# Performance work log

Hardware: AMD Instinct MI355X
Metric: run time of the kernel (lower is better)

## Reference

```python
import jax, jax.numpy as jnp
import numpy as np

N_HEAD, D_HEAD = 16, 64
D_MODEL = N_HEAD * D_HEAD
QLEN, MLEN, BSZ = 1024, 1024, 4
KLEN = QLEN + MLEN
LN_EPS = 1e-5


def setup_inputs() -> dict:
    key = jax.random.key(0)
    ks = jax.random.split(key, 8)
    w = jax.random.normal(ks[0], (QLEN, BSZ, D_MODEL), jnp.float32)
    r = jax.random.normal(ks[1], (KLEN, D_MODEL), jnp.float32)
    mems = jax.random.normal(ks[2], (MLEN, BSZ, D_MODEL), jnp.float32)
    # causal mask over (qlen, klen): query i may attend keys j <= i + MLEN
    i = jnp.arange(QLEN)[:, None]
    j = jnp.arange(KLEN)[None, :]
    attn_mask = j > (i + MLEN)  # True = masked
    s = 1.0 / np.sqrt(D_MODEL)
    qkv_w = jax.random.normal(ks[3], (3 * D_MODEL, D_MODEL), jnp.float32) * s
    r_net_w = jax.random.normal(ks[4], (D_MODEL, D_MODEL), jnp.float32) * s
    o_w = jax.random.normal(ks[5], (D_MODEL, D_MODEL), jnp.float32) * s
    r_r_bias = jax.random.normal(ks[6], (N_HEAD, D_HEAD), jnp.float32) * 0.02
    r_w_bias = jax.random.normal(ks[7], (N_HEAD, D_HEAD), jnp.float32) * 0.02
    ln_gamma = jnp.ones((D_MODEL,), jnp.float32)
    ln_beta = jnp.zeros((D_MODEL,), jnp.float32)
    return {"w": w, "r": r, "mems": mems, "attn_mask": attn_mask,
            "qkv_w": qkv_w, "r_net_w": r_net_w, "o_w": o_w,
            "r_r_bias": r_r_bias, "r_w_bias": r_w_bias,
            "ln_gamma": ln_gamma, "ln_beta": ln_beta}


def _layer_norm(x, g, b):
    mu = jnp.mean(x, axis=-1, keepdims=True)
    var = jnp.var(x, axis=-1, keepdims=True)
    return (x - mu) * jax.lax.rsqrt(var + LN_EPS) * g + b


def _rel_shift(x):
    # x: [qlen, rlen, bsz, n_head]
    q, rl, b, n = x.shape
    x_pad = jnp.pad(x, ((0, 0), (1, 0), (0, 0), (0, 0)))  # zero row at front of axis 1
    x_pad = x_pad.reshape(rl + 1, q, b, n)
    return x_pad[1:].reshape(q, rl, b, n)


def reference(w, r, mems, attn_mask, qkv_w, r_net_w, o_w, r_r_bias, r_w_bias, ln_gamma, ln_beta):
    qlen, bsz = w.shape[0], w.shape[1]
    cat = jnp.concatenate([mems, w], axis=0)  # [klen, b, d]
    klen = cat.shape[0]
    w_heads = cat @ qkv_w.T  # [klen, b, 3*d]
    r_head_k = (r @ r_net_w.T).reshape(r.shape[0], N_HEAD, D_HEAD)  # [rlen, n, dh]
    w_q, w_k, w_v = jnp.split(w_heads, 3, axis=-1)
    w_q = w_q[-qlen:].reshape(qlen, bsz, N_HEAD, D_HEAD)
    w_k = w_k.reshape(klen, bsz, N_HEAD, D_HEAD)
    w_v = w_v.reshape(klen, bsz, N_HEAD, D_HEAD)

    scale = 1.0 / np.sqrt(D_HEAD)
    AC = jnp.einsum('ibnd,jbnd->ijbn', w_q + r_w_bias, w_k)
    BD = _rel_shift(jnp.einsum('ibnd,jnd->ijbn', w_q + r_r_bias, r_head_k))
    attn_score = (AC + BD) * scale
    attn_score = jnp.where(attn_mask[None, :, :, None].transpose(1, 2, 0, 3), -1e30, attn_score) if False else \
        jnp.where(attn_mask[:, :, None, None], jnp.float32(-1e30), attn_score)
    attn_prob = jax.nn.softmax(attn_score, axis=1)
    attn_vec = jnp.einsum('ijbn,jbnd->ibnd', attn_prob, w_v)
    attn_vec = attn_vec.reshape(qlen, bsz, N_HEAD * D_HEAD)
    attn_out = attn_vec @ o_w.T
    return _layer_norm(w + attn_out, ln_gamma, ln_beta)
```

## Files before the change

kernel.cpp:

```cpp
#include <hip/hip_runtime.h>
#include <hip/hip_bf16.h>

typedef __attribute__((ext_vector_type(8))) short short8;
typedef __attribute__((ext_vector_type(4))) float f32x4;
typedef __hip_bfloat16 bf16;

#define NHEAD 16
#define DHEAD 64
#define DMODEL 1024
#define QLEN 1024
#define MLEN 1024
#define BSZ 4
#define KLEN 2048
#define LOG2E 1.44269504088896f

__device__ __forceinline__ float fast_exp2(float x) {
#if __has_builtin(__builtin_amdgcn_exp2f)
  return __builtin_amdgcn_exp2f(x);
#else
  return exp2f(x);
#endif
}

__device__ __forceinline__ short8 ld8(const bf16* p) { return *(const short8*)p; }
__device__ __forceinline__ void st8(bf16* p, short8 v) { *(short8*)p = v; }
__device__ __forceinline__ f32x4 mfma16(short8 a, short8 b, f32x4 c) {
  return __builtin_amdgcn_mfma_f32_16x16x32_bf16(a, b, c, 0, 0, 0);
}
__device__ __forceinline__ float bfu2f(unsigned short u) {
  unsigned int x = ((unsigned int)u) << 16;
  return __uint_as_float(x);
}
__device__ __forceinline__ unsigned short f2bfu(float f) {
  bf16 t = __float2bfloat16(f);
  return *(unsigned short*)&t;
}
__device__ __forceinline__ unsigned short f2bfu_fast(float f) {
  return (unsigned short)((__float_as_uint(f) + 0x8000u) >> 16);
}
__device__ __forceinline__ bf16 bf16_raw(unsigned short u) {
  bf16 t; *(unsigned short*)&t = u; return t;
}
__device__ __forceinline__ void async16(const bf16* g, bf16* l) {
  __builtin_amdgcn_global_load_lds(
      (const __attribute__((address_space(1))) unsigned int*)g,
      (__attribute__((address_space(3))) unsigned int*)l, 16, 0, 0);
}

#define DPPF(x, ctrl, rm) \
  __int_as_float(__builtin_amdgcn_update_dpp( \
      __float_as_int(x), __float_as_int(x), (ctrl), (rm), 0xF, false))

__global__ void detect_dtype(const unsigned short* wq, int* flag) {
  const int tid = threadIdx.x;
  int cnt = 0;
  #pragma unroll
  for (int j = 0; j < 8; ++j) {
    unsigned short u = wq[2 * (tid * 8 + j)];
    int e = (u >> 7) & 0xFF;
    if (e >= 100 && e <= 134) cnt++;
  }
  #pragma unroll
  for (int o = 32; o > 0; o >>= 1) cnt += __shfl_xor(cnt, o, 64);
  __shared__ int red[4];
  if ((tid & 63) == 0) red[tid >> 6] = cnt;
  __syncthreads();
  if (tid == 0) {
    int total = red[0] + red[1] + red[2] + red[3];
    *flag = (total > 1024) ? 0 : 1;
  }
}

__global__ __launch_bounds__(256) void convert_inputs(
    const void* s0, const void* s1, const void* s2,
    const void* s3, const void* s4, const void* s5,
    bf16* d0, bf16* d1, bf16* d2, bf16* d3, bf16* d4, bf16* d5,
    const int* flag)
{
  const int b = blockIdx.x;
  const void* src; bf16* dst; int lb;
  if (b < 2048)      { src = s0; dst = d0; lb = b; }
  else if (b < 4096) { src = s1; dst = d1; lb = b - 2048; }
  else if (b < 5120) { src = s2; dst = d2; lb = b - 4096; }
  else if (b < 6656) { src = s3; dst = d3; lb = b - 5120; }
  else if (b < 7168) { src = s4; dst = d4; lb = b - 6656; }
  else               { src = s5; dst = d5; lb = b - 7168; }
  const size_t idx = ((size_t)lb * 256 + threadIdx.x) * 8;
  if (*flag) {
    const float* f = (const float*)src;
    short8 v;
    #pragma unroll
    for (int j = 0; j < 8; ++j) v[j] = (short)f2bfu(f[idx + j]);
    st8(dst + idx, v);
  } else {
    st8(dst + idx, ld8((const bf16*)src + idx));
  }
}

__device__ __forceinline__ void gemm_core64(
    const bf16* const ap[4], const bf16* const bp[4],
    bf16* As, bf16* Bs, int wv, int wm, int wn, int lr, int lg,
    f32x4 acc[4][4])
{
  const int sx = lr & 7;
  for (int k0 = 0; k0 < DMODEL; k0 += 64) {
    #pragma unroll
    for (int p = 0; p < 4; ++p) {
      async16(ap[p] + k0, As + (wv * 32 + p * 8) * 64);
      async16(bp[p] + k0, Bs + (wv * 32 + p * 8) * 64);
    }
    __syncthreads();
    #pragma unroll
    for (int ks = 0; ks < 2; ++ks) {
      const int col = (((ks * 4 + lg) ^ sx) << 3);
      short8 af[4], bfr[4];
      #pragma unroll
      for (int mt = 0; mt < 4; ++mt) af[mt] = ld8(As + (wm * 64 + mt * 16 + lr) * 64 + col);
      #pragma unroll
      for (int nt = 0; nt < 4; ++nt) bfr[nt] = ld8(Bs + (wn * 64 + nt * 16 + lr) * 64 + col);
      #pragma unroll
      for (int mt = 0; mt < 4; ++mt)
        #pragma unroll
        for (int nt = 0; nt < 4; ++nt)
          acc[mt][nt] = mfma16(af[mt], bfr[nt], acc[mt][nt]);
    }
    __syncthreads();
  }
}

__global__ __launch_bounds__(256) void qkv_gemm(
    const bf16* __restrict__ w, const bf16* __restrict__ mems,
    const bf16* __restrict__ qkv_w,
    const bf16* __restrict__ r, const bf16* __restrict__ rnet_w,
    const void* __restrict__ r_w_bias, const void* __restrict__ r_r_bias,
    const int* __restrict__ flag,
    bf16* __restrict__ qac, bf16* __restrict__ qbd,
    bf16* __restrict__ kbuf, bf16* __restrict__ vbuf,
    bf16* __restrict__ rkbuf)
{
  const int id = blockIdx.x;
  int sec, bx, by;
  if (id < 256)       { sec = 0; bx = id >> 5;                    by = 32 + (id & 31); }
  else if (id < 768)  { sec = 1; int t = id - 256;  bx = 8  + (t >> 6); by = t & 63; }
  else if (id < 1280) { sec = 2; int t = id - 768;  bx = 16 + (t >> 6); by = t & 63; }
  else                { sec = 3; int t = id - 1280; bx = 24 + (t >> 4); by = t & 15; }
  __shared__ bf16 sh[16384];
  bf16* As = sh;
  bf16* Bs = sh + 8192;
  const int tid = threadIdx.x;
  const int lane = tid & 63, wv = tid >> 6;
  const int wm = wv >> 1, wn = wv & 1;
  const int lr = lane & 15, lg = lane >> 4;
  const int lr8 = lane >> 3;
  const int ucol = ((lane & 7) ^ lr8) * 8;
  const bf16 *ap[4], *bp[4];
  #pragma unroll
  for (int p = 0; p < 4; ++p) {
    int arow = wv * 32 + p * 8 + lr8;
    if (sec == 3) {
      ap[p] = r + (size_t)(by * 128 + arow) * DMODEL + ucol;
      bp[p] = rnet_w + (size_t)((bx - 24) * 128 + arow) * DMODEL + ucol;
    } else {
      int m = by * 128 + arow;
      int j = m >> 2, b = m & 3;
      ap[p] = ((j < MLEN) ? (mems + ((size_t)(j * BSZ + b)) * DMODEL)
                          : (w + ((size_t)((j - MLEN) * BSZ + b)) * DMODEL)) + ucol;
      bp[p] = qkv_w + (size_t)(bx * 128 + arow) * DMODEL + ucol;
    }
  }
  f32x4 zero = {0.f, 0.f, 0.f, 0.f};
  f32x4 acc[4][4];
  #pragma unroll
  for (int a = 0; a < 4; ++a)
    #pragma unroll
    for (int c2 = 0; c2 < 4; ++c2) acc[a][c2] = zero;
  gemm_core64(ap, bp, As, Bs, wv, wm, wn, lr, lg, acc);

  if (sec == 2) {
    #pragma unroll
    for (int nt = 0; nt < 4; ++nt) {
      int n = wn * 64 + nt * 16 + lr;
      #pragma unroll
      for (int mt = 0; mt < 4; ++mt) {
        int jl = wm * 16 + mt * 4 + lg;
        #pragma unroll
        for (int rr = 0; rr < 4; ++rr) {
          int x = rr * 32 + jl;
          sh[n * 128 + (((x >> 4) ^ (n & 7)) << 4) + (x & 15)] =
              __float2bfloat16(acc[mt][nt][rr]);
        }
      }
    }
    __syncthreads();
    const int grp = lane >> 3, sl = lane & 7;
    const int hbase = (bx - 16) * 2;
    #pragma unroll
    for (int i = 0; i < 16; ++i) {
      int idx = i * 32 + wv * 8 + grp;
      int n = idx >> 2, bb = idx & 3;
      int x0 = bb * 32 + sl * 4;
      ushort4 v4 = *(const ushort4*)(sh + n * 128 + (((x0 >> 4) ^ (n & 7)) << 4) + (x0 & 15));
      int hh = hbase + (n >> 6), dd = n & 63;
      *(ushort4*)(vbuf + ((size_t)(bb * NHEAD + hh) * DHEAD + dd) * KLEN + by * 32 + sl * 4) = v4;
    }
    return;
  }
  if (sec == 3) {
    #pragma unroll
    for (int nt = 0; nt < 4; ++nt) {
      int col = (bx - 24) * 128 + wn * 64 + nt * 16 + lr;
      int h = col >> 6, d = col & 63;
      #pragma unroll
      for (int mt = 0; mt < 4; ++mt) {
        #pragma unroll
        for (int rr = 0; rr < 4; ++rr) {
          int m = by * 128 + wm * 64 + mt * 16 + lg * 4 + rr;
          rkbuf[((size_t)h * KLEN + m) * DHEAD + d] = __float2bfloat16(acc[mt][nt][rr]);
        }
      }
    }
    return;
  }
  const int isf = (sec == 0) ? *flag : 0;
  const float QSC = 0.125f * LOG2E;
  #pragma unroll
  for (int nt = 0; nt < 4; ++nt) {
    int col = bx * 128 + wn * 64 + nt * 16 + lr;
    int nn = col & 1023;
    int h = nn >> 6, d = nn & 63;
    float rwb = 0.f, rrb = 0.f;
    if (sec == 0) {
      if (isf) { rwb = ((const float*)r_w_bias)[nn]; rrb = ((const float*)r_r_bias)[nn]; }
      else { rwb = __bfloat162float(((const bf16*)r_w_bias)[nn]);
             rrb = __bfloat162float(((const bf16*)r_r_bias)[nn]); }
    }
    #pragma unroll
    for (int mt = 0; mt < 4; ++mt) {
      #pragma unroll
      for (int rr = 0; rr < 4; ++rr) {
        int m = by * 128 + wm * 64 + mt * 16 + lg * 4 + rr;
        int j = m >> 2, b = m & 3;
        float v = acc[mt][nt][rr];
        if (sec == 0) {
          int i = j - MLEN;
          size_t base = (((size_t)(b * NHEAD + h)) * QLEN + i) * DHEAD + d;
          qac[base] = __float2bfloat16((v + rwb) * QSC);
          qbd[base] = __float2bfloat16((v + rrb) * QSC);
        } else {
          kbuf[(((size_t)(b * NHEAD + h)) * KLEN + j) * DHEAD + d] = __float2bfloat16(v);
        }
      }
    }
  }
}

#define RRBODY(RR, CTRL) { \
    const int di = g * 4 + RR; \
    float sh[5]; \
    _Pragma("unroll") for (int ct = 0; ct < 5; ++ct) { \
      float y = Gr[ct][RR]; \
      sh[ct] = __int_as_float(__builtin_amdgcn_update_dpp( \
          __float_as_int(y), __float_as_int(y), (CTRL), 0xF, 0xF, false)); \
    } \
    float sv[4]; \
    _Pragma("unroll") for (int jt = 0; jt < 4; ++jt) { \
      float bd = (c > di) ? sh[jt + 1] : sh[jt]; \
      sv[jt] = S[jt][RR] + bd; \
    } \
    if (lastt) { \
      const int ig = i0 + wv * 16 + di; \
      _Pragma("unroll") for (int jt = 0; jt < 4; ++jt) \
        if (j0 + jt * 16 + c > ig + MLEN) sv[jt] = -1e30f; \
    } \
    _Pragma("unroll") for (int jt = 0; jt < 4; ++jt) { \
      float pv = fast_exp2(sv[jt]); \
      ls[RR] += pv; \
      pw[di * 64 + ((((jt * 2) + (c >> 3)) ^ (di & 7)) << 3) + (c & 7)] = \
          bf16_raw(f2bfu_fast(pv)); \
    } \
  }

__global__ __launch_bounds__(256, 4) void attn_kernel(
    const bf16* __restrict__ qac, const bf16* __restrict__ qbd,
    const bf16* __restrict__ kbuf, const bf16* __restrict__ vbuf,
    const bf16* __restrict__ rkbuf, bf16* __restrict__ av)
{
  const int id = blockIdx.x;
  const int qt = 15 - (id >> 6);
  const int bh = id & 63;
  const int b = bh >> 4, h = bh & 15;
  const int i0 = qt * 64;
  __shared__ bf16 Ks[64 * 64];
  __shared__ bf16 Vt[64 * 64];
  __shared__ bf16 Rs[128 * 64];
  __shared__ bf16 Ps[4 * 16 * 64];
  const int tid = threadIdx.x;
  const int wv = tid >> 6, lane = tid & 63;
  const int c = lane & 15, g = lane >> 4;
  const size_t bhb = (size_t)(b * NHEAD + h);
  const int lr8 = lane >> 3;
  const int ucol = ((lane & 7) ^ lr8) * 8;
  const int sw0 = ((0 + g) ^ (c & 7)) * 8;
  const int sw1 = ((4 + g) ^ (c & 7)) * 8;

  short8 qaf[2], qbf[2];
  {
    const size_t qrow = (bhb * QLEN + i0 + wv * 16 + c) * DHEAD;
    #pragma unroll
    for (int ks = 0; ks < 2; ++ks) {
      qaf[ks] = ld8(qac + qrow + ks * 32 + g * 8);
      qbf[ks] = ld8(qbd + qrow + ks * 32 + g * 8);
    }
  }
  f32x4 zero = {0.f, 0.f, 0.f, 0.f};
  f32x4 O[4];
  #pragma unroll
  for (int dt = 0; dt < 4; ++dt) O[dt] = zero;
  float ls[4] = {0.f, 0.f, 0.f, 0.f};

  bf16* pw = Ps + wv * (16 * 64);
  const bf16* kc = Ks + c * 64;
  const bf16* vc = Vt + c * 64;
  const bf16* rc = Rs + (c + 48 - wv * 16) * 64;
  const int ntiles = qt + 17;
  for (int t = 0; t < ntiles; ++t) {
    const int j0 = t * 64;
    const int m_lo = j0 - i0 + 960;
    #pragma unroll
    for (int p = 0; p < 2; ++p) {
      int r0 = wv * 16 + p * 8;
      async16(kbuf + (bhb * KLEN + j0 + r0 + lr8) * DHEAD + ucol, Ks + r0 * 64);
      async16(vbuf + (bhb * DHEAD + r0 + lr8) * KLEN + j0 + ucol, Vt + r0 * 64);
    }
    #pragma unroll
    for (int p = 0; p < 4; ++p) {
      int r0 = wv * 32 + p * 8;
      async16(rkbuf + ((size_t)h * KLEN + m_lo + r0 + lr8) * DHEAD + ucol, Rs + r0 * 64);
    }
    __syncthreads();
    f32x4 S[4], G[5];
    #pragma unroll
    for (int jt = 0; jt < 4; ++jt) S[jt] = zero;
    #pragma unroll
    for (int ct = 0; ct < 5; ++ct) G[ct] = zero;
    #pragma unroll
    for (int ks = 0; ks < 2; ++ks) {
      const int sw = ks ? sw1 : sw0;
      #pragma unroll
      for (int jt = 0; jt < 4; ++jt)
        S[jt] = mfma16(qaf[ks], ld8(kc + jt * 1024 + sw), S[jt]);
      #pragma unroll
      for (int ct = 0; ct < 5; ++ct)
        G[ct] = mfma16(qbf[ks], ld8(rc + ct * 1024 + sw), G[ct]);
    }
    float Gr[5][4];
    #pragma unroll
    for (int ct = 0; ct < 5; ++ct)
      #pragma unroll
      for (int rr = 0; rr < 4; ++rr) {
        float y = G[ct][rr];
        y = DPPF(y, 0x124, 0xE);
        y = DPPF(y, 0x124, 0xC);
        y = DPPF(y, 0x124, 0x8);
        Gr[ct][rr] = y;
      }
    const bool lastt = (t == ntiles - 1);
    RRBODY(0, 0x121)
    RRBODY(1, 0x122)
    RRBODY(2, 0x123)
    RRBODY(3, 0x124)
    #pragma unroll
    for (int ks = 0; ks < 2; ++ks) {
      short8 pf = ld8(pw + c * 64 + (((ks * 4 + g) ^ (c & 7)) << 3));
      const int sw = ks ? sw1 : sw0;
      #pragma unroll
      for (int dt = 0; dt < 4; ++dt)
        O[dt] = mfma16(pf, ld8(vc + dt * 1024 + sw), O[dt]);
    }
    __syncthreads();
  }
  #pragma unroll
  for (int rr = 0; rr < 4; ++rr) {
    float s = ls[rr];
    s += DPPF(s, 0xB1, 0xF);
    s += DPPF(s, 0x4E, 0xF);
    s += DPPF(s, 0x141, 0xF);
    s += DPPF(s, 0x140, 0xF);
    ls[rr] = s;
  }
  #pragma unroll
  for (int rr = 0; rr < 4; ++rr) {
    float inv = 1.0f / ls[rr];
    #pragma unroll
    for (int dt = 0; dt < 4; ++dt) {
      int ig = i0 + wv * 16 + g * 4 + rr;
      int d = dt * 16 + c;
      av[((size_t)ig * BSZ + b) * DMODEL + h * DHEAD + d] =
          __float2bfloat16(O[dt][rr] * inv);
    }
  }
}

__global__ __launch_bounds__(256) void out_gemm(
    const bf16* __restrict__ av, const bf16* __restrict__ o_w,
    bf16* __restrict__ ao)
{
  const int id = blockIdx.x;
  const int bx = id >> 5, by = id & 31;
  __shared__ bf16 As[128 * 64];
  __shared__ bf16 Bs[128 * 64];
  const int tid = threadIdx.x;
  const int lane = tid & 63, wv = tid >> 6;
  const int wm = wv >> 1, wn = wv & 1;
  const int lr = lane & 15, lg = lane >> 4;
  const int lr8 = lane >> 3;
  const int ucol = ((lane & 7) ^ lr8) * 8;
  const bf16 *ap[4], *bp[4];
  #pragma unroll
  for (int p = 0; p < 4; ++p) {
    int arow = wv * 32 + p * 8 + lr8;
    ap[p] = av + (size_t)(by * 128 + arow) * DMODEL + ucol;
    bp[p] = o_w + (size_t)(bx * 128 + arow) * DMODEL + ucol;
  }
  f32x4 zero = {0.f, 0.f, 0.f, 0.f};
  f32x4 acc[4][4];
  #pragma unroll
  for (int a = 0; a < 4; ++a)
    #pragma unroll
    for (int c2 = 0; c2 < 4; ++c2) acc[a][c2] = zero;
  gemm_core64(ap, bp, As, Bs, wv, wm, wn, lr, lg, acc);
  #pragma unroll
  for (int nt = 0; nt < 4; ++nt) {
    int col = bx * 128 + wn * 64 + nt * 16 + lr;
    #pragma unroll
    for (int mt = 0; mt < 4; ++mt) {
      #pragma unroll
      for (int rr = 0; rr < 4; ++rr) {
        int m = by * 128 + wm * 64 + mt * 16 + lg * 4 + rr;
        ao[(size_t)m * DMODEL + col] = __float2bfloat16(acc[mt][nt][rr]);
      }
    }
  }
}

__global__ __launch_bounds__(256) void ln_kernel(
    const void* __restrict__ wz, const bf16* __restrict__ ao,
    const void* __restrict__ gz, const void* __restrict__ bz,
    void* __restrict__ outz, const int* __restrict__ flag)
{
  const int m = blockIdx.x;
  const int tid = threadIdx.x;
  const int isf = *flag;
  ushort4 au = ((const ushort4*)ao)[m * 256 + tid];
  float a4[4];
  a4[0] = bfu2f(au.x); a4[1] = bfu2f(au.y); a4[2] = bfu2f(au.z); a4[3] = bfu2f(au.w);
  float x[4], gg[4], bb[4];
  if (isf) {
    f32x4 w4 = ((const f32x4*)wz)[m * 256 + tid];
    f32x4 g4 = ((const f32x4*)gz)[tid];
    f32x4 b4 = ((const f32x4*)bz)[tid];
    #pragma unroll
    for (int k = 0; k < 4; ++k) { x[k] = w4[k] + a4[k]; gg[k] = g4[k]; bb[k] = b4[k]; }
  } else {
    ushort4 w4 = ((const ushort4*)wz)[m * 256 + tid];
    ushort4 g4 = ((const ushort4*)gz)[tid];
    ushort4 b4 = ((const ushort4*)bz)[tid];
    x[0] = bfu2f(w4.x) + a4[0]; x[1] = bfu2f(w4.y) + a4[1];
    x[2] = bfu2f(w4.z) + a4[2]; x[3] = bfu2f(w4.w) + a4[3];
    gg[0] = bfu2f(g4.x); gg[1] = bfu2f(g4.y); gg[2] = bfu2f(g4.z); gg[3] = bfu2f(g4.w);
    bb[0] = bfu2f(b4.x); bb[1] = bfu2f(b4.y); bb[2] = bfu2f(b4.z); bb[3] = bfu2f(b4.w);
  }
  float s = x[0] + x[1] + x[2] + x[3];
  float s2 = x[0]*x[0] + x[1]*x[1] + x[2]*x[2] + x[3]*x[3];
  #pragma unroll
  for (int o = 32; o > 0; o >>= 1) {
    s += __shfl_xor(s, o, 64);
    s2 += __shfl_xor(s2, o, 64);
  }
  __shared__ float red[8];
  const int wv = tid >> 6, lane = tid & 63;
  if (lane == 0) { red[wv] = s; red[4 + wv] = s2; }
  __syncthreads();
  s = red[0] + red[1] + red[2] + red[3];
  s2 = red[4] + red[5] + red[6] + red[7];
  const float mu = s * (1.0f / DMODEL);
  const float var = s2 * (1.0f / DMODEL) - mu * mu;
  const float rstd = rsqrtf(var + 1e-5f);
  float y[4];
  #pragma unroll
  for (int k = 0; k < 4; ++k) y[k] = (x[k] - mu) * rstd * gg[k] + bb[k];
  if (isf) {
    f32x4 o4; o4[0] = y[0]; o4[1] = y[1]; o4[2] = y[2]; o4[3] = y[3];
    ((f32x4*)outz)[m * 256 + tid] = o4;
  } else {
    ushort4 o4;
    o4.x = f2bfu(y[0]); o4.y = f2bfu(y[1]); o4.z = f2bfu(y[2]); o4.w = f2bfu(y[3]);
    ((ushort4*)outz)[m * 256 + tid] = o4;
  }
}

extern "C" void kernel_launch(void* const* d_in, const int* in_sizes, int n_in,
                              void* d_out, int out_size, void* d_ws, size_t ws_size,
                              hipStream_t stream) {
  (void)in_sizes; (void)n_in; (void)out_size; (void)ws_size;
  const void* w      = d_in[0];
  const void* r      = d_in[1];
  const void* mems   = d_in[2];
  const void* qkv_w  = d_in[4];
  const void* rnet_w = d_in[5];
  const void* o_w    = d_in[6];
  const void* rrb    = d_in[7];
  const void* rwb    = d_in[8];
  const void* ln_g   = d_in[9];
  const void* ln_b   = d_in[10];

  char* ws = (char*)d_ws;
  const size_t MB = 1ull << 20;
  bf16* cw    = (bf16*)(ws + 0 * MB);
  bf16* cmems = (bf16*)(ws + 8 * MB);
  bf16* cr    = (bf16*)(ws + 16 * MB);
  bf16* cqkvw = (bf16*)(ws + 20 * MB);
  bf16* crnet = (bf16*)(ws + 26 * MB);
  bf16* cow   = (bf16*)(ws + 28 * MB);
  int*  flag  = (int*)(ws + 30 * MB);
  bf16* qac   = (bf16*)(ws + 31 * MB);
  bf16* qbd   = (bf16*)(ws + 39 * MB);
  bf16* kbuf  = (bf16*)(ws + 47 * MB);
  bf16* vbuf  = (bf16*)(ws + 63 * MB);
  bf16* rkbuf = (bf16*)(ws + 79 * MB);
  bf16* av    = (bf16*)(ws + 83 * MB);
  bf16* ao    = (bf16*)(ws + 0 * MB);

  detect_dtype<<<1, 256, 0, stream>>>((const unsigned short*)w, flag);
  convert_inputs<<<7680, 256, 0, stream>>>(w, mems, r, qkv_w, rnet_w, o_w,
                                           cw, cmems, cr, cqkvw, crnet, cow, flag);
  qkv_gemm<<<1408, 256, 0, stream>>>(cw, cmems, cqkvw, cr, crnet,
                                     rwb, rrb, flag,
                                     qac, qbd, kbuf, vbuf, rkbuf);
  attn_kernel<<<1024, 256, 0, stream>>>(qac, qbd, kbuf, vbuf, rkbuf, av);
  out_gemm<<<256, 256, 0, stream>>>(av, cow, ao);
  ln_kernel<<<dim3(4096), 256, 0, stream>>>(w, ao, ln_g, ln_b, d_out, flag);
}
```

Baseline: 307.0 us.

## Reuse overlapping R tile via ring buffer and overlap R loads with QK MFMAs

The relative-position R window slides by 64 rows per key tile, so the loop now keeps 128 rows in LDS as a ring indexed by an XOR offset. After the first tile it loads only the 64 new rows, and the wait on them is moved so the QK MFMAs run while they arrive. The DPP row-shift chain is cut from three steps to two, and the fp32→bf16 convert uses vector loads. The cost is more complex waitcnt/barrier handling and a split MFMA phase with an extra barrier.

New measurement: 299.9 us. -2.3%, faster.

```diff
diff --git a/kernel.cpp b/kernel.cpp
--- a/kernel.cpp
+++ b/kernel.cpp
@@ -87,10 +87,14 @@
   else               { src = s5; dst = d5; lb = b - 7168; }
   const size_t idx = ((size_t)lb * 256 + threadIdx.x) * 8;
   if (*flag) {
-    const float* f = (const float*)src;
+    const f32x4* f = (const f32x4*)src;
+    f32x4 a = f[idx >> 2];
+    f32x4 c = f[(idx >> 2) + 1];
     short8 v;
-    #pragma unroll
-    for (int j = 0; j < 8; ++j) v[j] = (short)f2bfu(f[idx + j]);
+    v[0] = (short)f2bfu(a[0]); v[1] = (short)f2bfu(a[1]);
+    v[2] = (short)f2bfu(a[2]); v[3] = (short)f2bfu(a[3]);
+    v[4] = (short)f2bfu(c[0]); v[5] = (short)f2bfu(c[1]);
+    v[6] = (short)f2bfu(c[2]); v[7] = (short)f2bfu(c[3]);
     st8(dst + idx, v);
   } else {
     st8(dst + idx, ld8((const bf16*)src + idx));
@@ -321,23 +325,45 @@
   bf16* pw = Ps + wv * (16 * 64);
   const bf16* kc = Ks + c * 64;
   const bf16* vc = Vt + c * 64;
-  const bf16* rc = Rs + (c + 48 - wv * 16) * 64;
+  const int relb = c + 48 - wv * 16;
+  int relo[2][5];
+  #pragma unroll
+  for (int ks = 0; ks < 2; ++ks)
+    #pragma unroll
+    for (int ct = 0; ct < 5; ++ct)
+      relo[ks][ct] = (relb + ct * 16) * 64 + (ks ? sw1 : sw0);
+
   const int ntiles = qt + 17;
+  int roff = ((15 - qt) & 1) << 6;
   for (int t = 0; t < ntiles; ++t) {
     const int j0 = t * 64;
     const int m_lo = j0 - i0 + 960;
+    const int ro = roff << 6;
     #pragma unroll
     for (int p = 0; p < 2; ++p) {
       int r0 = wv * 16 + p * 8;
       async16(kbuf + (bhb * KLEN + j0 + r0 + lr8) * DHEAD + ucol, Ks + r0 * 64);
       async16(vbuf + (bhb * DHEAD + r0 + lr8) * KLEN + j0 + ucol, Vt + r0 * 64);
     }
-    #pragma unroll
-    for (int p = 0; p < 4; ++p) {
-      int r0 = wv * 32 + p * 8;
-      async16(rkbuf + ((size_t)h * KLEN + m_lo + r0 + lr8) * DHEAD + ucol, Rs + r0 * 64);
-    }
-    __syncthreads();
+    if (t == 0) {
+      #pragma unroll
+      for (int p = 0; p < 4; ++p) {
+        int r0 = wv * 32 + p * 8;
+        async16(rkbuf + ((size_t)h * KLEN + m_lo + r0 + lr8) * DHEAD + ucol,
+                Rs + ((r0 << 6) ^ ro));
+      }
+      asm volatile("s_waitcnt vmcnt(4)" ::: "memory");
+    } else {
+      #pragma unroll
+      for (int p = 0; p < 2; ++p) {
+        int r1 = 64 + wv * 16 + p * 8;
+        async16(rkbuf + ((size_t)h * KLEN + m_lo + r1 + lr8) * DHEAD + ucol,
+                Rs + ((r1 << 6) ^ ro));
+      }
+      asm volatile("s_waitcnt vmcnt(2)" ::: "memory");
+    }
+    __builtin_amdgcn_s_barrier();
+    __builtin_amdgcn_sched_barrier(0);
     f32x4 S[4], G[5];
     #pragma unroll
     for (int jt = 0; jt < 4; ++jt) S[jt] = zero;
@@ -349,9 +375,15 @@
       #pragma unroll
       for (int jt = 0; jt < 4; ++jt)
         S[jt] = mfma16(qaf[ks], ld8(kc + jt * 1024 + sw), S[jt]);
+    }
+    __builtin_amdgcn_sched_barrier(0);
+    asm volatile("s_waitcnt vmcnt(0)" ::: "memory");
+    __syncthreads();
+    #pragma unroll
+    for (int ks = 0; ks < 2; ++ks) {
       #pragma unroll
       for (int ct = 0; ct < 5; ++ct)
-        G[ct] = mfma16(qbf[ks], ld8(rc + ct * 1024 + sw), G[ct]);
+        G[ct] = mfma16(qbf[ks], ld8(Rs + (relo[ks][ct] ^ ro)), G[ct]);
     }
     float Gr[5][4];
     #pragma unroll
@@ -359,9 +391,8 @@
       #pragma unroll
       for (int rr = 0; rr < 4; ++rr) {
         float y = G[ct][rr];
-        y = DPPF(y, 0x124, 0xE);
-        y = DPPF(y, 0x124, 0xC);
-        y = DPPF(y, 0x124, 0x8);
+        y = DPPF(y, 0x124, 0xA);
+        y = DPPF(y, 0x128, 0xC);
         Gr[ct][rr] = y;
       }
     const bool lastt = (t == ntiles - 1);
@@ -378,6 +409,7 @@
         O[dt] = mfma16(pf, ld8(vc + dt * 1024 + sw), O[dt]);
     }
     __syncthreads();
+    roff ^= 64;
   }
   #pragma unroll
   for (int rr = 0; rr < 4; ++rr) {
```
